# Kernel optimization log

Measured on AMD Instinct MI355X. Metric: run time of the kernel, lower is better.

Reference implementation:

```python
import jax, jax.numpy as jnp
import numpy as np

D_IN = 1024
D_OUT = 1024
NUM_HEADS = 16
HEAD_DIM = D_OUT // NUM_HEADS


def setup_inputs() -> dict:
    key = jax.random.key(0)
    ks = jax.random.split(key, 6)
    b, T = 2, 2048
    scale = 0.02
    x = jax.random.normal(ks[0], (b, T, D_IN), dtype=jnp.float32)
    Wq = jax.random.normal(ks[1], (D_IN, D_OUT), dtype=jnp.float32) * scale
    Wk = jax.random.normal(ks[2], (D_IN, D_OUT), dtype=jnp.float32) * scale
    Wv = jax.random.normal(ks[3], (D_IN, D_OUT), dtype=jnp.float32) * scale
    Wo = jax.random.normal(ks[4], (D_OUT, D_OUT), dtype=jnp.float32) * scale
    bo = jnp.zeros((D_OUT,), dtype=jnp.float32)
    return {"x": x, "Wq": Wq, "Wk": Wk, "Wv": Wv, "Wo": Wo, "bo": bo}


def reference(x, Wq, Wk, Wv, Wo, bo):
    b, T, _ = x.shape
    H, Dh = NUM_HEADS, HEAD_DIM
    # projections: [b,T,d_out] -> [b,H,T,Dh]
    q = (x @ Wq).reshape(b, T, H, Dh).transpose(0, 2, 1, 3)
    k = (x @ Wk).reshape(b, T, H, Dh).transpose(0, 2, 1, 3)
    v = (x @ Wv).reshape(b, T, H, Dh).transpose(0, 2, 1, 3)
    # scores: [b,H,T,T]
    att = jnp.einsum('bhqd,bhkd->bhqk', q, k)
    causal = jnp.triu(jnp.ones((T, T), dtype=bool), k=1)
    att = jnp.where(causal, -jnp.inf, att)
    att = jax.nn.softmax(att / np.sqrt(Dh).astype(np.float32), axis=-1)
    # dropout p=0.0 -> identity
    y = jnp.einsum('bhqk,bhkd->bhqd', att, v)
    y = y.transpose(0, 2, 1, 3).reshape(b, T, H * Dh)
    return y @ Wo + bo
```

## Files before the change

### kernel.cpp

```cpp
#include <hip/hip_runtime.h>

#define T_   2048
#define DM   1024
#define H_   16
#define DH   64

typedef unsigned short u16;
typedef unsigned int u32;
typedef __attribute__((ext_vector_type(8))) short bf16x8;
typedef __attribute__((ext_vector_type(8))) unsigned short u16x8;
typedef __attribute__((ext_vector_type(4))) float f32x4;
typedef __attribute__((ext_vector_type(16))) float f32x16;
typedef __attribute__((ext_vector_type(2))) unsigned int u32x2;

static __device__ __forceinline__ u16 f2b(float f) {
  unsigned int u = __builtin_bit_cast(unsigned int, f);
  u += 0x7fff + ((u >> 16) & 1);
  return (u16)(u >> 16);
}

static __device__ __forceinline__ u32 cvtpk(float a, float b) {
  u32 d;
  asm("v_cvt_pk_bf16_f32 %0, %1, %2" : "=v"(d) : "v"(a), "v"(b));
  return d;
}

static __device__ __forceinline__ void gll16(const void* g, void* l) {
  __builtin_amdgcn_global_load_lds(
      (const __attribute__((address_space(1))) unsigned int*)g,
      (__attribute__((address_space(3))) unsigned int*)l, 16, 0, 0);
}

__global__ __launch_bounds__(256) void k_cvt(
    const float* __restrict__ x, u16* __restrict__ xb,
    const float* __restrict__ Wq, const float* __restrict__ Wk,
    const float* __restrict__ Wv, const float* __restrict__ Wo,
    u16* __restrict__ oq, u16* __restrict__ ok, u16* __restrict__ ov,
    u16* __restrict__ oo) {
  __shared__ u16 tile[64][65];
  const int z = blockIdx.z;
  if (z == 4) {
    const int b = blockIdx.y * 16 + blockIdx.x;
#pragma unroll
    for (int it = 0; it < 8; ++it) {
      const int i = b * 16384 + it * 2048 + threadIdx.x * 8;
      float4 a = *(const float4*)(x + i);
      float4 c = *(const float4*)(x + i + 4);
      u16x8 r;
      r[0] = f2b(a.x); r[1] = f2b(a.y); r[2] = f2b(a.z); r[3] = f2b(a.w);
      r[4] = f2b(c.x); r[5] = f2b(c.y); r[6] = f2b(c.z); r[7] = f2b(c.w);
      *(u16x8*)(xb + i) = r;
    }
    return;
  }
  const float* W; u16* Wt;
  if (z == 0)      { W = Wq; Wt = oq; }
  else if (z == 1) { W = Wk; Wt = ok; }
  else if (z == 2) { W = Wv; Wt = ov; }
  else             { W = Wo; Wt = oo; }
  const float wsc = (z == 0) ? 0.1803368801111204f : 1.0f;
  int k0 = blockIdx.x * 64, n0 = blockIdx.y * 64;
  int r = threadIdx.x >> 2, c0 = (threadIdx.x & 3) * 16;
  const float* src = W + (k0 + r) * DM + n0 + c0;
#pragma unroll
  for (int e = 0; e < 16; e += 4) {
    float4 v = *(const float4*)(src + e);
    tile[r][c0 + e + 0] = f2b(v.x * wsc);
    tile[r][c0 + e + 1] = f2b(v.y * wsc);
    tile[r][c0 + e + 2] = f2b(v.z * wsc);
    tile[r][c0 + e + 3] = f2b(v.w * wsc);
  }
  __syncthreads();
  u16x8 a, b;
#pragma unroll
  for (int e = 0; e < 8; ++e) a[e] = tile[c0 + e][r];
#pragma unroll
  for (int e = 0; e < 8; ++e) b[e] = tile[c0 + 8 + e][r];
  u16* dst = Wt + (n0 + r) * DM + k0 + c0;
  *(u16x8*)dst = a;
  *(u16x8*)(dst + 8) = b;
}

__global__ __launch_bounds__(256) void k_qkv(
    const u16* __restrict__ X, const u16* __restrict__ Wqt,
    const u16* __restrict__ Wkt, const u16* __restrict__ Wvt,
    u16* __restrict__ Qg, u16* __restrict__ Kg, u16* __restrict__ Vtg) {
  __shared__ char smem[34816];
  const int tid = threadIdx.x, lane = tid & 63, w = tid >> 6;
  const int frow = lane & 15, fk = lane >> 4;
  const int wr = (w >> 1) * 64, wc = (w & 1) * 64;
  const int m0 = blockIdx.x * 128;
  const int by = blockIdx.y;
  const int z = by >> 3, n0 = (by & 7) * 128;
  const u16* Wt = (z == 0) ? Wqt : (z == 1) ? Wkt : Wvt;
  const u16* Ap = X + m0 * DM;
  const u16* Bp = Wt + n0 * DM;
  const int sro = lane >> 2;
  const int sce = ((lane & 3) ^ ((lane >> 3) & 3)) << 3;

  f32x4 acc[4][4];
#pragma unroll
  for (int mi = 0; mi < 4; ++mi)
#pragma unroll
    for (int ni = 0; ni < 4; ++ni) acc[mi][ni] = (f32x4){0.f, 0.f, 0.f, 0.f};

#define STAGEJ(K0, BUF)                                                      \
  _Pragma("unroll") for (int c = 0; c < 2; ++c) {                            \
    const int g = w + c * 4;                          \
    gll16(Ap + (g * 16 + sro) * DM + (K0) + sce, (BUF) + g * 1024);          \
    gll16(Bp + (g * 16 + sro) * DM + (K0) + sce, (BUF) + 8192 + g * 1024);   \
  }

  STAGEJ(0, smem)
  asm volatile("s_waitcnt vmcnt(0)" ::: "memory");
  __syncthreads();

  for (int j = 0; j < 32; ++j) {
    char* cur = smem + (j & 1) * 16384;
    char* nxt = smem + ((j + 1) & 1) * 16384;
    if (j < 31) { STAGEJ((j + 1) * 32, nxt) }
    bf16x8 a[4], b[4];
#pragma unroll
    for (int mi = 0; mi < 4; ++mi) {
      const int rho = wr + mi * 16 + frow;
      a[mi] = *(const bf16x8*)(cur + rho * 64 + ((fk ^ ((rho >> 1) & 3)) << 4));
    }
#pragma unroll
    for (int ni = 0; ni < 4; ++ni) {
      const int rho = wc + ni * 16 + frow;
      b[ni] = *(const bf16x8*)(cur + 8192 + rho * 64 +
                               ((fk ^ ((rho >> 1) & 3)) << 4));
    }
    __builtin_amdgcn_s_setprio(1);
#pragma unroll
    for (int mi = 0; mi < 4; ++mi)
#pragma unroll
      for (int ni = 0; ni < 4; ++ni)
        acc[mi][ni] = __builtin_amdgcn_mfma_f32_16x16x32_bf16(
            a[mi], b[ni], acc[mi][ni], 0, 0, 0);
    __builtin_amdgcn_s_setprio(0);
    __syncthreads();
  }
#undef STAGEJ

  if (z < 2) {
    u16* out = (z == 0) ? Qg : Kg;
#pragma unroll
    for (int mi = 0; mi < 4; ++mi)
#pragma unroll
      for (int ni = 0; ni < 4; ++ni)
#pragma unroll
        for (int r = 0; r < 4; ++r) {
          int m = m0 + wr + mi * 16 + fk * 4 + r;
          int nl = n0 + wc + ni * 16 + frow;
          int b = m >> 11, t = m & 2047, h = nl >> 6, d = nl & 63;
          out[((b * H_ + h) * T_ + t) * DH + d] = f2b(acc[mi][ni][r]);
        }
  } else {
    u16* Tl = (u16*)smem;
#pragma unroll
    for (int ni = 0; ni < 4; ++ni) {
      const int n = wc + ni * 16 + frow;
#pragma unroll
      for (int mi = 0; mi < 4; ++mi)
#pragma unroll
        for (int r = 0; r < 4; ++r)
          Tl[n * 136 + wr + mi * 16 + fk * 4 + r] = f2b(acc[mi][ni][r]);
    }
    __syncthreads();
    const int n = tid >> 1, c0 = (tid & 1) * 64;
    const int ng = n0 + n, h = ng >> 6, d = ng & 63;
    const int b = m0 >> 11;
    const int tb = (m0 & 2047) + c0;
    u16* dst = Vtg + ((b * H_ + h) * DH + d) * T_ + tb;
#pragma unroll
    for (int e = 0; e < 8; ++e)
      *(u16x8*)(dst + e * 8) = *(const u16x8*)(Tl + n * 136 + c0 + e * 8);
  }
}

static __device__ __forceinline__ bf16x8 ldf(const char* base, int rho,
                                             int k16) {
  return *(const bf16x8*)(base + rho * 128 + ((k16 ^ (rho & 7)) << 4));
}

__global__ __launch_bounds__(256) void k_out(
    const u16* __restrict__ Y, const u16* __restrict__ Wot,
    const float* __restrict__ bo, float* __restrict__ out) {
  __shared__ char smem[24576];
  char* As = smem;
  char* Bs = smem + 8192;
  const int tid = threadIdx.x, lane = tid & 63, w = tid >> 6;
  const int frow = lane & 15, fk = lane >> 4;
  const int wr = (w >> 1) * 32, wc = (w & 1) * 64;
  const int m0 = blockIdx.x * 64, n0 = blockIdx.y * 128;
  const u16* Ap = Y + m0 * DM;
  const u16* Bp = Wot + n0 * DM;
  const int ro = lane >> 3;
  const int ce = ((lane & 7) ^ ro) << 3;

  f32x4 acc[2][4];
#pragma unroll
  for (int mi = 0; mi < 2; ++mi)
#pragma unroll
    for (int ni = 0; ni < 4; ++ni) acc[mi][ni] = (f32x4){0.f, 0.f, 0.f, 0.f};

  for (int k0 = 0; k0 < DM; k0 += 64) {
#pragma unroll
    for (int c = 0; c < 2; ++c) {
      const int g8 = (w * 2 + c) * 8;
      gll16(Ap + (g8 + ro) * DM + k0 + ce, As + g8 * 128);
    }
#pragma unroll
    for (int c = 0; c < 4; ++c) {
      const int g8 = (w * 4 + c) * 8;
      gll16(Bp + (g8 + ro) * DM + k0 + ce, Bs + g8 * 128);
    }
    asm volatile("s_waitcnt vmcnt(0)" ::: "memory");
    __syncthreads();
    bf16x8 a[2][2], b[4][2];
#pragma unroll
    for (int mi = 0; mi < 2; ++mi)
#pragma unroll
      for (int kk = 0; kk < 2; ++kk)
        a[mi][kk] = ldf(As, wr + mi * 16 + frow, kk * 4 + fk);
#pragma unroll
    for (int ni = 0; ni < 4; ++ni)
#pragma unroll
      for (int kk = 0; kk < 2; ++kk)
        b[ni][kk] = ldf(Bs, wc + ni * 16 + frow, kk * 4 + fk);
#pragma unroll
    for (int mi = 0; mi < 2; ++mi)
#pragma unroll
      for (int ni = 0; ni < 4; ++ni)
#pragma unroll
        for (int kk = 0; kk < 2; ++kk)
          acc[mi][ni] = __builtin_amdgcn_mfma_f32_16x16x32_bf16(
              a[mi][kk], b[ni][kk], acc[mi][ni], 0, 0, 0);
    __syncthreads();
  }
#pragma unroll
  for (int mi = 0; mi < 2; ++mi)
#pragma unroll
    for (int ni = 0; ni < 4; ++ni)
#pragma unroll
      for (int r = 0; r < 4; ++r) {
        int m = m0 + wr + mi * 16 + fk * 4 + r;
        int n = n0 + wc + ni * 16 + frow;
        out[m * DM + n] = acc[mi][ni][r] + bo[n];
      }
}

__global__ __launch_bounds__(256) void k_attn(
    const u16* __restrict__ Qg, const u16* __restrict__ Kg,
    const u16* __restrict__ Vtg, u16* __restrict__ Yg) {
  __shared__ char smem[33792];
  const int bh = blockIdx.x;
  const int qt = 63 - blockIdx.y;
  const int q0 = qt * 32;
  const int tid = threadIdx.x, w = tid >> 6, lane = tid & 63;
  const int hi = lane >> 5, qq = lane & 31;
  const u16* Qb = Qg + bh * (T_ * DH);
  const u16* Kb = Kg + bh * (T_ * DH);
  const u16* Vb = Vtg + bh * (DH * T_);
  const int qrow = q0 + qq;
  char* Wb = smem + w * 8192;
  float* lpb = (float*)(smem + 32768);

  bf16x8 qf[4];
#pragma unroll
  for (int kb = 0; kb < 4; ++kb)
    qf[kb] = *(const bf16x8*)(Qb + qrow * DH + kb * 16 + hi * 8);

  f32x16 o0, o1;
#pragma unroll
  for (int r = 0; r < 16; ++r) { o0[r] = 0.f; o1[r] = 0.f; }
  float lp = 0.f;

  const int nt = (qt >> 1) + 1;
  const int ro = lane >> 3;
  const int ce = ((lane & 7) ^ ro) << 3;

  if (w < nt) {
#pragma unroll
    for (int g = 0; g < 8; ++g)
      gll16(Kb + (w * 64 + g * 8 + ro) * DH + ce, Wb + g * 1024);

    for (int t = w; t < nt; t += 4) {
      asm volatile("s_waitcnt vmcnt(0)" ::: "memory");
      bf16x8 kf[8];
#pragma unroll
      for (int kb = 0; kb < 4; ++kb) {
        kf[kb] = *(const bf16x8*)(
            Wb + qq * 128 + (((kb * 2 + hi) ^ (qq & 7)) << 4));
        kf[4 + kb] = *(const bf16x8*)(
            Wb + (qq + 32) * 128 + (((kb * 2 + hi) ^ (qq & 7)) << 4));
      }
      asm volatile("s_waitcnt lgkmcnt(0)" ::: "memory");
#pragma unroll
      for (int g = 0; g < 8; ++g)
        gll16(Vb + (g * 8 + ro) * T_ + t * 64 + ce, Wb + g * 1024);
      f32x16 s0, s1;
#pragma unroll
      for (int r = 0; r < 16; ++r) { s0[r] = 0.f; s1[r] = 0.f; }
      __builtin_amdgcn_s_setprio(1);
#pragma unroll
      for (int kb = 0; kb < 4; ++kb) {
        s0 = __builtin_amdgcn_mfma_f32_32x32x16_bf16(kf[kb], qf[kb], s0, 0, 0, 0);
        s1 = __builtin_amdgcn_mfma_f32_32x32x16_bf16(kf[4 + kb], qf[kb], s1, 0, 0, 0);
      }
      __builtin_amdgcn_s_setprio(0);
      if (t == nt - 1) {
        const int j0 = t * 64;
#pragma unroll
        for (int r = 0; r < 16; ++r) {
          const int cr = j0 + (r & 3) + 8 * (r >> 2) + 4 * hi;
          if (cr > qrow) s0[r] = -1e30f;
          if (cr + 32 > qrow) s1[r] = -1e30f;
        }
      }
      float ts[16];
#pragma unroll
      for (int r = 0; r < 16; ++r) {
        s0[r] = __builtin_amdgcn_exp2f(s0[r] - 16.0f);
        s1[r] = __builtin_amdgcn_exp2f(s1[r] - 16.0f);
        ts[r] = s0[r] + s1[r];
      }
#pragma unroll
      for (int stp = 8; stp > 0; stp >>= 1)
#pragma unroll
        for (int r = 0; r < stp; ++r) ts[r] += ts[r + stp];
      lp += ts[0];
      bf16x8 pb[4];
#define MKCH(DST, S, RB)                                                     \
  {                                                                          \
    u32 a01 = cvtpk(S[RB + 0], S[RB + 1]);                                   \
    u32 a23 = cvtpk(S[RB + 2], S[RB + 3]);                                   \
    u32 a45 = cvtpk(S[RB + 4], S[RB + 5]);                                   \
    u32 a67 = cvtpk(S[RB + 6], S[RB + 7]);                                   \
    asm volatile("v_permlane32_swap_b32 %0, %1" : "+v"(a01), "+v"(a45));     \
    asm volatile("v_permlane32_swap_b32 %0, %1" : "+v"(a23), "+v"(a67));     \
    u32x4_t t4;                                                              \
    t4[0] = a01; t4[1] = a23; t4[2] = a45; t4[3] = a67;                      \
    DST = __builtin_bit_cast(bf16x8, t4);                                    \
  }
      typedef __attribute__((ext_vector_type(4))) unsigned int u32x4_t;
      MKCH(pb[0], s0, 0)
      MKCH(pb[1], s0, 8)
      MKCH(pb[2], s1, 0)
      MKCH(pb[3], s1, 8)
#undef MKCH
      asm volatile("s_waitcnt vmcnt(0)" ::: "memory");
      bf16x8 vf[8];
#pragma unroll
      for (int jc = 0; jc < 4; ++jc) {
        vf[jc] = *(const bf16x8*)(
            Wb + qq * 128 + (((jc * 2 + hi) ^ (qq & 7)) << 4));
        vf[4 + jc] = *(const bf16x8*)(
            Wb + (qq + 32) * 128 + (((jc * 2 + hi) ^ (qq & 7)) << 4));
      }
      asm volatile("s_waitcnt lgkmcnt(0)" ::: "memory");
      if (t + 4 < nt) {
#pragma unroll
        for (int g = 0; g < 8; ++g)
          gll16(Kb + ((t + 4) * 64 + g * 8 + ro) * DH + ce, Wb + g * 1024);
      }
      __builtin_amdgcn_s_setprio(1);
#pragma unroll
      for (int jc = 0; jc < 4; ++jc) {
        o0 = __builtin_amdgcn_mfma_f32_32x32x16_bf16(vf[jc], pb[jc], o0, 0, 0, 0);
        o1 = __builtin_amdgcn_mfma_f32_32x32x16_bf16(vf[4 + jc], pb[jc], o1, 0, 0, 0);
      }
      __builtin_amdgcn_s_setprio(0);
    }
  }

  asm volatile("s_waitcnt vmcnt(0)" ::: "memory");
  float* po = (float*)Wb;
#pragma unroll
  for (int r = 0; r < 16; ++r) {
    po[r * 64 + lane] = o0[r];
    po[(16 + r) * 64 + lane] = o1[r];
  }
  lpb[w * 64 + lane] = lp;
  __syncthreads();
  if (w == 0) {
#pragma unroll
    for (int sw = 1; sw < 4; ++sw) {
      const float* ps = (const float*)(smem + sw * 8192);
      lp += lpb[sw * 64 + lane];
#pragma unroll
      for (int r = 0; r < 16; ++r) {
        o0[r] += ps[r * 64 + lane];
        o1[r] += ps[(16 + r) * 64 + lane];
      }
    }
    lp += __shfl_xor(lp, 32);
    const float rl = 1.0f / lp;
    const int obase = ((bh >> 4) * T_ + qrow) * DM + (bh & 15) * DH;
#pragma unroll
    for (int g = 0; g < 4; ++g) {
      u32x2 st;
      st[0] = cvtpk(o0[g * 4 + 0] * rl, o0[g * 4 + 1] * rl);
      st[1] = cvtpk(o0[g * 4 + 2] * rl, o0[g * 4 + 3] * rl);
      *(u32x2*)(Yg + obase + g * 8 + hi * 4) = st;
      st[0] = cvtpk(o1[g * 4 + 0] * rl, o1[g * 4 + 1] * rl);
      st[1] = cvtpk(o1[g * 4 + 2] * rl, o1[g * 4 + 3] * rl);
      *(u32x2*)(Yg + obase + 32 + g * 8 + hi * 4) = st;
    }
  }
}


extern "C" void kernel_launch(void* const* d_in, const int* in_sizes, int n_in,
                              void* d_out, int out_size, void* d_ws,
                              size_t ws_size, hipStream_t stream) {
  const float* x  = (const float*)d_in[0];
  const float* Wq = (const float*)d_in[1];
  const float* Wk = (const float*)d_in[2];
  const float* Wv = (const float*)d_in[3];
  const float* Wo = (const float*)d_in[4];
  const float* bo = (const float*)d_in[5];
  float* out = (float*)d_out;
  char* ws = (char*)d_ws;

  u16* xb  = (u16*)(ws);
  u16* wqt = (u16*)(ws + (8ull << 20));
  u16* wkt = (u16*)(ws + (10ull << 20));
  u16* wvt = (u16*)(ws + (12ull << 20));
  u16* wot = (u16*)(ws + (14ull << 20));
  u16* Qg  = (u16*)(ws + (16ull << 20));
  u16* Kg  = (u16*)(ws + (24ull << 20));
  u16* Vtg = (u16*)(ws + (32ull << 20));
  u16* Yg  = (u16*)(ws + (40ull << 20));

  k_cvt<<<dim3(16, 16, 5), 256, 0, stream>>>(x, xb, Wq, Wk, Wv, Wo,
                                             wqt, wkt, wvt, wot);
  k_qkv<<<dim3(32, 24), 256, 0, stream>>>(xb, wqt, wkt, wvt, Qg, Kg, Vtg);
  k_attn<<<dim3(32, 64), 256, 0, stream>>>(Qg, Kg, Vtg, Yg);
  k_out<<<dim3(64, 8), 256, 0, stream>>>(Yg, wot, bo, out);
}
```

Baseline: 108.8 us.

## Double-buffer output projection GEMM and defer softmax row-sum after PV MFMAs

The output-projection kernel now uses K=32 tiles with two LDS buffers, prefetching the next tile while MFMAs run on the current one. This removes the full vmcnt wait before each compute step, and the kernel raises wave priority around the MFMA block. The price is twice as many loop iterations and barriers, plus a new XOR swizzle for the smaller tile. In the attention kernel, the reduction of the softmax row sum is moved after the PV MFMA issue so the VALU adds can overlap with matrix work.

After: 109.5 us. About the same (+0.7%).

```diff
diff --git a/kernel.cpp b/kernel.cpp
--- a/kernel.cpp
+++ b/kernel.cpp
@@ -179,25 +179,18 @@
   }
 }
 
-static __device__ __forceinline__ bf16x8 ldf(const char* base, int rho,
-                                             int k16) {
-  return *(const bf16x8*)(base + rho * 128 + ((k16 ^ (rho & 7)) << 4));
-}
-
 __global__ __launch_bounds__(256) void k_out(
     const u16* __restrict__ Y, const u16* __restrict__ Wot,
     const float* __restrict__ bo, float* __restrict__ out) {
   __shared__ char smem[24576];
-  char* As = smem;
-  char* Bs = smem + 8192;
   const int tid = threadIdx.x, lane = tid & 63, w = tid >> 6;
   const int frow = lane & 15, fk = lane >> 4;
   const int wr = (w >> 1) * 32, wc = (w & 1) * 64;
   const int m0 = blockIdx.x * 64, n0 = blockIdx.y * 128;
   const u16* Ap = Y + m0 * DM;
   const u16* Bp = Wot + n0 * DM;
-  const int ro = lane >> 3;
-  const int ce = ((lane & 7) ^ ro) << 3;
+  const int sro = lane >> 2;
+  const int sce = ((lane & 3) ^ ((lane >> 3) & 3)) << 3;
 
   f32x4 acc[2][4];
 #pragma unroll
@@ -205,40 +198,47 @@
 #pragma unroll
     for (int ni = 0; ni < 4; ++ni) acc[mi][ni] = (f32x4){0.f, 0.f, 0.f, 0.f};
 
-  for (int k0 = 0; k0 < DM; k0 += 64) {
-#pragma unroll
-    for (int c = 0; c < 2; ++c) {
-      const int g8 = (w * 2 + c) * 8;
-      gll16(Ap + (g8 + ro) * DM + k0 + ce, As + g8 * 128);
-    }
-#pragma unroll
-    for (int c = 0; c < 4; ++c) {
-      const int g8 = (w * 4 + c) * 8;
-      gll16(Bp + (g8 + ro) * DM + k0 + ce, Bs + g8 * 128);
-    }
-    asm volatile("s_waitcnt vmcnt(0)" ::: "memory");
+#define STAGEO(K0, BUF)                                                      \
+  {                                                                          \
+    gll16(Ap + (w * 16 + sro) * DM + (K0) + sce, (BUF) + w * 1024);          \
+    _Pragma("unroll") for (int c = 0; c < 2; ++c) {                          \
+      const int g = w + c * 4;                                               \
+      gll16(Bp + (g * 16 + sro) * DM + (K0) + sce, (BUF) + 4096 + g * 1024); \
+    }                                                                        \
+  }
+
+  STAGEO(0, smem)
+  asm volatile("s_waitcnt vmcnt(0)" ::: "memory");
+  __syncthreads();
+
+  for (int j = 0; j < 32; ++j) {
+    char* cur = smem + (j & 1) * 12288;
+    char* nxt = smem + ((j + 1) & 1) * 12288;
+    if (j < 31) { STAGEO((j + 1) * 32, nxt) }
+    bf16x8 a[2], b[4];
+#pragma unroll
+    for (int mi = 0; mi < 2; ++mi) {
+      const int rho = wr + mi * 16 + frow;
+      a[mi] = *(const bf16x8*)(cur + rho * 64 + ((fk ^ ((rho >> 1) & 3)) << 4));
+    }
+#pragma unroll
+    for (int ni = 0; ni < 4; ++ni) {
+      const int rho = wc + ni * 16 + frow;
+      b[ni] = *(const bf16x8*)(cur + 4096 + rho * 64 +
+                               ((fk ^ ((rho >> 1) & 3)) << 4));
+    }
+    __builtin_amdgcn_s_setprio(1);
+#pragma unroll
+    for (int mi = 0; mi < 2; ++mi)
+#pragma unroll
+      for (int ni = 0; ni < 4; ++ni)
+        acc[mi][ni] = __builtin_amdgcn_mfma_f32_16x16x32_bf16(
+            a[mi], b[ni], acc[mi][ni], 0, 0, 0);
+    __builtin_amdgcn_s_setprio(0);
     __syncthreads();
-    bf16x8 a[2][2], b[4][2];
-#pragma unroll
-    for (int mi = 0; mi < 2; ++mi)
-#pragma unroll
-      for (int kk = 0; kk < 2; ++kk)
-        a[mi][kk] = ldf(As, wr + mi * 16 + frow, kk * 4 + fk);
-#pragma unroll
-    for (int ni = 0; ni < 4; ++ni)
-#pragma unroll
-      for (int kk = 0; kk < 2; ++kk)
-        b[ni][kk] = ldf(Bs, wc + ni * 16 + frow, kk * 4 + fk);
-#pragma unroll
-    for (int mi = 0; mi < 2; ++mi)
-#pragma unroll
-      for (int ni = 0; ni < 4; ++ni)
-#pragma unroll
-        for (int kk = 0; kk < 2; ++kk)
-          acc[mi][ni] = __builtin_amdgcn_mfma_f32_16x16x32_bf16(
-              a[mi][kk], b[ni][kk], acc[mi][ni], 0, 0, 0);
-    __syncthreads();
-  }
+  }
+#undef STAGEO
+
 #pragma unroll
   for (int mi = 0; mi < 2; ++mi)
 #pragma unroll
@@ -326,11 +326,6 @@
         s1[r] = __builtin_amdgcn_exp2f(s1[r] - 16.0f);
         ts[r] = s0[r] + s1[r];
       }
-#pragma unroll
-      for (int stp = 8; stp > 0; stp >>= 1)
-#pragma unroll
-        for (int r = 0; r < stp; ++r) ts[r] += ts[r + stp];
-      lp += ts[0];
       bf16x8 pb[4];
 #define MKCH(DST, S, RB)                                                     \
   {                                                                          \
@@ -372,6 +367,11 @@
         o1 = __builtin_amdgcn_mfma_f32_32x32x16_bf16(vf[4 + jc], pb[jc], o1, 0, 0, 0);
       }
       __builtin_amdgcn_s_setprio(0);
+#pragma unroll
+      for (int stp = 8; stp > 0; stp >>= 1)
+#pragma unroll
+        for (int r = 0; r < stp; ++r) ts[r] += ts[r + stp];
+      lp += ts[0];
     }
   }
 
```
